# Kernel optimization log

Hardware: AMD Instinct MI355X
Metric: run time of the kernel (lower is better)

The kernel has to match this reference:

```python
import jax, jax.numpy as jnp
import numpy as np

N = 50000      # nodes
E = 800000     # edges (before self-loops)
IN = 256       # input_dim
HID = 72       # hidden_dim
HEADS = 4
NEG_SLOPE = 0.2  # PyG GATConv default leaky-relu slope


def setup_inputs() -> dict:
    key = jax.random.key(0)
    ks = jax.random.split(key, 16)
    rn = lambda k, shape: jax.random.normal(k, shape, jnp.float32) * 0.05
    return {
        "x": jax.random.normal(ks[0], (N, IN), jnp.float32),
        "edge_index": jax.random.randint(ks[1], (2, E), 0, N),
        "W_in": rn(ks[2], (IN, HID)), "b_in": jnp.zeros((HID,), jnp.float32),
        "W1": rn(ks[3], (HID, HEADS * HID)),
        "a_src1": rn(ks[4], (HEADS, HID)), "a_dst1": rn(ks[5], (HEADS, HID)),
        "b1": jnp.zeros((HEADS * HID,), jnp.float32),
        "W2": rn(ks[6], (HEADS * HID, HID)),
        "a_src2": rn(ks[7], (1, HID)), "a_dst2": rn(ks[8], (1, HID)),
        "b2": jnp.zeros((HID,), jnp.float32),
        "W3": rn(ks[9], (HID, HID)),
        "a_src3": rn(ks[10], (1, HID)), "a_dst3": rn(ks[11], (1, HID)),
        "b3": jnp.zeros((HID,), jnp.float32),
        "Ws1": rn(ks[12], (HID, 32)), "bs1": jnp.zeros((32,), jnp.float32),
        "Ws2": rn(ks[13], (32, 1)), "bs2": jnp.zeros((1,), jnp.float32),
    }


def gat_conv(x, src, dst, W, a_src, a_dst, bias, concat):
    # PyG GATConv (eval mode): per-head linear, leaky-relu attention logits,
    # segment softmax over incoming edges per destination, scatter-aggregate.
    H, C = a_src.shape
    h = (x @ W).reshape(-1, H, C)                      # [N, H, C]
    logit_s = jnp.einsum('nhc,hc->nh', h, a_src)       # [N, H]
    logit_d = jnp.einsum('nhc,hc->nh', h, a_dst)       # [N, H]
    e = jax.nn.leaky_relu(logit_s[src] + logit_d[dst], NEG_SLOPE)   # [Et, H]
    emax = jax.ops.segment_max(e, dst, num_segments=N)
    emax = jnp.where(jnp.isfinite(emax), emax, 0.0)
    p = jnp.exp(e - emax[dst])
    denom = jax.ops.segment_sum(p, dst, num_segments=N)
    alpha = p / jnp.maximum(denom[dst], 1e-16)         # [Et, H]
    out = jax.ops.segment_sum(h[src] * alpha[:, :, None], dst, num_segments=N)
    out = out.reshape(-1, H * C) if concat else out.mean(axis=1)
    return out + bias


def reference(x, edge_index, W_in, b_in,
              W1, a_src1, a_dst1, b1,
              W2, a_src2, a_dst2, b2,
              W3, a_src3, a_dst3, b3,
              Ws1, bs1, Ws2, bs2):
    loops = jnp.arange(N)                              # PyG add_self_loops=True
    src = jnp.concatenate([edge_index[0], loops])
    dst = jnp.concatenate([edge_index[1], loops])
    x0 = x @ W_in + b_in                               # [N, HID]
    h = jax.nn.elu(gat_conv(x0, src, dst, W1, a_src1, a_dst1, b1, True))
    h = jax.nn.elu(gat_conv(h, src, dst, W2, a_src2, a_dst2, b2, False))
    h = jax.nn.elu(gat_conv(h, src, dst, W3, a_src3, a_dst3, b3, False))
    h = h + x0
    score = jax.nn.relu(h @ Ws1 + bs1) @ Ws2 + bs2     # dropout = identity (eval)
    return score.squeeze(-1)                           # [N]
```

## Files before the change

### kernel.cpp

```cpp
#include <hip/hip_runtime.h>
#include <hip/hip_fp16.h>
#include <cmath>

#define NN 50000
#define EE 800000
#define ET (EE + NN)
#define IN_DIM 256
#define HID 72
#define CAP 96
#define NRANGE 8
#define RSPAN (NN / NRANGE)
#define SLICE_E 8192

typedef __attribute__((ext_vector_type(8))) short s8v;
typedef __attribute__((ext_vector_type(4))) short s4v;
typedef __attribute__((ext_vector_type(4))) float f4v;
typedef __attribute__((ext_vector_type(2))) float f2v;

__device__ __forceinline__ ushort f2bf(float x) {
    uint u = __float_as_uint(x);
    return (ushort)((u + 0x7fffu + ((u >> 16) & 1u)) >> 16);
}
__device__ __forceinline__ float bf2f(ushort h) {
    return __uint_as_float(((uint)h) << 16);
}
__device__ __forceinline__ void split4(const float4& v, s4v& h, s4v& l) {
    ushort h0 = f2bf(v.x), h1 = f2bf(v.y), h2 = f2bf(v.z), h3 = f2bf(v.w);
    h = (s4v){(short)h0, (short)h1, (short)h2, (short)h3};
    l = (s4v){(short)f2bf(v.x - bf2f(h0)), (short)f2bf(v.y - bf2f(h1)),
              (short)f2bf(v.z - bf2f(h2)), (short)f2bf(v.w - bf2f(h3))};
}
__device__ __forceinline__ f4v mfma16(s8v a, s8v b, f4v c) {
    return __builtin_amdgcn_mfma_f32_16x16x32_bf16(a, b, c, 0, 0, 0);
}
__device__ __forceinline__ f2v unpack_h2(uint pv) {
    __half2 hv = __builtin_bit_cast(__half2, pv);
    return (f2v){__low2float(hv), __high2float(hv)};
}
__device__ __forceinline__ uint pack_h2(float a, float b) {
    __half2 hp = __floats2half2_rn(a, b);
    return __builtin_bit_cast(uint, hp);
}
__device__ __forceinline__ f2v fma2(float w, f2v c, f2v a) {
    return __builtin_elementwise_fma((f2v){w, w}, c, a);
}

__device__ __forceinline__ void wsplit_one(const float* W, int ldw, int K,
        int idx, short* outH, short* outL) {
    int h = idx / (72 * K);
    int rem = idx - h * 72 * K;
    int n = rem / K, k = rem - n * K;
    float v = W[(size_t)k * ldw + h * 72 + n];
    ushort hi = f2bf(v);
    outH[idx] = (short)hi;
    outL[idx] = (short)f2bf(v - bf2f(hi));
}

#define PR0 18432
#define PR1 (PR0 + 20736)
#define PR2 (PR1 + 20736)
#define PR3 (PR2 + 5184)
#define PR4 (PR3 + 288)
#define PRTOT (PR4 + NN)

__global__ __launch_bounds__(256) void prep_kernel(
        const float* __restrict__ W_in, const float* __restrict__ W1,
        const float* __restrict__ W2, const float* __restrict__ W3,
        const float* __restrict__ a_src, const float* __restrict__ a_dst,
        short* __restrict__ BtInH, short* __restrict__ BtInL,
        short* __restrict__ Bt1H, short* __restrict__ Bt1L,
        short* __restrict__ Bt2H, short* __restrict__ Bt2L,
        short* __restrict__ Bt3H, short* __restrict__ Bt3L,
        float* __restrict__ wsrc, float* __restrict__ wdst,
        int* __restrict__ deg, ushort* __restrict__ ell) {
    int gid = blockIdx.x * 256 + threadIdx.x;
    if (gid < PR0) {
        wsplit_one(W_in, 72, 256, gid, BtInH, BtInL);
    } else if (gid < PR1) {
        wsplit_one(W1, 288, 72, gid - PR0, Bt1H, Bt1L);
    } else if (gid < PR2) {
        wsplit_one(W2, 72, 288, gid - PR1, Bt2H, Bt2L);
    } else if (gid < PR3) {
        wsplit_one(W3, 72, 72, gid - PR2, Bt3H, Bt3L);
    } else if (gid < PR4) {
        int j = gid - PR3;
        int h = j / HID, k = j % HID;
        const float* wrow = W1 + (size_t)k * (4 * HID) + h * HID;
        const float* as = a_src + h * HID;
        const float* ad = a_dst + h * HID;
        float s = 0.f, d = 0.f;
        for (int c = 0; c < HID; ++c) {
            float w = wrow[c];
            s = fmaf(w, as[c], s);
            d = fmaf(w, ad[c], d);
        }
        wsrc[j] = s;
        wdst[j] = d;
    } else if (gid < PRTOT) {
        int i = gid - PR4;
        deg[i] = 1;
        ell[(size_t)i * CAP] = (ushort)i;
    }
}

template <int NLOGIT, bool ELU_EPI, bool BATCHED, bool PACKOUT, bool APACK, bool ADJ>
__global__ __launch_bounds__(256) void gemm_mfma(
        const void* __restrict__ Ain, const short* __restrict__ BtH,
        const short* __restrict__ BtL, const float* __restrict__ bias,
        float* __restrict__ C, uint* __restrict__ Cp, int ldp,
        const float* __restrict__ lvs, const float* __restrict__ lvd,
        float* __restrict__ ls, float* __restrict__ ld,
        int M, int K, int lda, int Nfull,
        const int* __restrict__ eiw, int* __restrict__ degw,
        ushort* __restrict__ ellw, int gemmBlocks) {
    __shared__ __align__(16) short AhS[64 * 40], AlS[64 * 40];
    __shared__ __align__(16) short BhS[80 * 40], BlS[80 * 40];

    int tid = threadIdx.x;

    if (ADJ && (int)blockIdx.x >= gemmBlocks) {
        int ab = blockIdx.x - gemmBlocks;
        int slice = ab >> 3;
        int range = blockIdx.x & 7;
        int lo = range * RSPAN;
        int hi = lo + RSPAN;
        #pragma unroll 2
        for (int j = 0; j < 8; ++j) {
            int i0 = slice * SLICE_E + j * 1024 + tid * 4;
            if (i0 >= EE) break;
            int4 d4 = *(const int4*)(eiw + EE + i0);
            int4 s4 = *(const int4*)(eiw + i0);
            int dd[4] = {d4.x, d4.y, d4.z, d4.w};
            int ss[4] = {s4.x, s4.y, s4.z, s4.w};
            #pragma unroll
            for (int u = 0; u < 4; ++u) {
                if (dd[u] >= lo && dd[u] < hi) {
                    int pos = atomicAdd(&degw[dd[u]], 1);
                    if (pos < CAP) ellw[(size_t)dd[u] * CAP + pos] = (ushort)ss[u];
                }
            }
        }
        return;
    }

    int row0 = blockIdx.x * 64;
    int hh = BATCHED ? blockIdx.y : 0;
    int aoff = BATCHED ? hh * (APACK ? 36 : 72) : 0;
    int coff = BATCHED ? hh * 72 : 0;
    const short* bhg = BtH + (size_t)hh * 72 * K;
    const short* blg = BtL + (size_t)hh * 72 * K;

    for (int i = tid; i < 8 * 40; i += 256) {
        BhS[72 * 40 + i] = 0;
        BlS[72 * 40 + i] = 0;
    }

    int w = tid >> 6;
    int lane = tid & 63;
    int q = lane >> 4, l16 = lane & 15;

    f4v acc[5];
    #pragma unroll
    for (int f = 0; f < 5; ++f) acc[f] = (f4v)0.f;

    int ar = tid >> 2;
    int aseg = tid & 3;
    bool arok = (row0 + ar) < M;
    const float* aptrf = nullptr;
    const uint*  aptru = nullptr;
    if constexpr (APACK) {
        aptru = (const uint*)Ain + (size_t)(row0 + ar) * lda + aoff;
    } else {
        aptrf = (const float*)Ain + (size_t)(row0 + ar) * lda + aoff;
    }
    int bn0 = tid >> 2, bq0 = tid & 3;
    int bn1 = (tid + 256) >> 2;

    float4 va, vb;
    s8v bh0, bl0, bh1, bl1;
    auto gload = [&](int k0) {
        va = (float4){0, 0, 0, 0};
        vb = (float4){0, 0, 0, 0};
        int ka = k0 + aseg * 8;
        if constexpr (APACK) {
            if (arok && ka < K) {
                uint4 u = *(const uint4*)(aptru + (ka >> 1));
                f2v p0 = unpack_h2(u.x), p1 = unpack_h2(u.y);
                f2v p2 = unpack_h2(u.z), p3 = unpack_h2(u.w);
                va = (float4){p0.x, p0.y, p1.x, p1.y};
                vb = (float4){p2.x, p2.y, p3.x, p3.y};
            }
        } else {
            if (arok && ka < K)     va = *(const float4*)(aptrf + ka);
            if (arok && ka + 4 < K) vb = *(const float4*)(aptrf + ka + 4);
        }
        bh0 = (s8v)0; bl0 = (s8v)0;
        int kb = k0 + bq0 * 8;
        if (kb < K) {
            bh0 = *(const s8v*)(bhg + (size_t)bn0 * K + kb);
            bl0 = *(const s8v*)(blg + (size_t)bn0 * K + kb);
        }
        bh1 = (s8v)0; bl1 = (s8v)0;
        if (tid < 32 && kb < K) {
            bh1 = *(const s8v*)(bhg + (size_t)bn1 * K + kb);
            bl1 = *(const s8v*)(blg + (size_t)bn1 * K + kb);
        }
    };
    auto commit = [&]() {
        s4v h0, l0, h1, l1;
        split4(va, h0, l0);
        split4(vb, h1, l1);
        *(s4v*)&AhS[ar * 40 + aseg * 8]     = h0;
        *(s4v*)&AhS[ar * 40 + aseg * 8 + 4] = h1;
        *(s4v*)&AlS[ar * 40 + aseg * 8]     = l0;
        *(s4v*)&AlS[ar * 40 + aseg * 8 + 4] = l1;
        *(s8v*)&BhS[bn0 * 40 + bq0 * 8] = bh0;
        *(s8v*)&BlS[bn0 * 40 + bq0 * 8] = bl0;
        if (tid < 32) {
            *(s8v*)&BhS[bn1 * 40 + bq0 * 8] = bh1;
            *(s8v*)&BlS[bn1 * 40 + bq0 * 8] = bl1;
        }
    };

    int ntiles = (K + 31) / 32;
    gload(0);
    for (int t = 0; t < ntiles; ++t) {
        commit();
        __syncthreads();
        if (t + 1 < ntiles) gload((t + 1) * 32);
        s8v ah = *(const s8v*)&AhS[(w * 16 + l16) * 40 + q * 8];
        s8v al = *(const s8v*)&AlS[(w * 16 + l16) * 40 + q * 8];
        #pragma unroll
        for (int f = 0; f < 5; ++f) {
            s8v bh = *(const s8v*)&BhS[(f * 16 + l16) * 40 + q * 8];
            s8v bl = *(const s8v*)&BlS[(f * 16 + l16) * 40 + q * 8];
            acc[f] = mfma16(ah, bh, acc[f]);
            acc[f] = mfma16(ah, bl, acc[f]);
            acc[f] = mfma16(al, bh, acc[f]);
        }
        __syncthreads();
    }

    float v[5][4];
    #pragma unroll
    for (int f = 0; f < 5; ++f) {
        int col = f * 16 + l16;
        bool cv = col < 72;
        #pragma unroll
        for (int r = 0; r < 4; ++r) {
            float t = acc[f][r];
            if (cv && bias) t += bias[coff + col];
            if (ELU_EPI) t = (t > 0.f) ? t : expm1f(t);
            v[f][r] = cv ? t : 0.f;
        }
    }
    if (NLOGIT > 0) {
        #pragma unroll
        for (int h2 = 0; h2 < NLOGIT; ++h2) {
            #pragma unroll
            for (int r = 0; r < 4; ++r) {
                float s = 0.f, d = 0.f;
                #pragma unroll
                for (int f = 0; f < 5; ++f) {
                    int col = f * 16 + l16;
                    float lw = (col < 72) ? lvs[h2 * 72 + col] : 0.f;
                    float dw = (col < 72) ? lvd[h2 * 72 + col] : 0.f;
                    s = fmaf(v[f][r], lw, s);
                    d = fmaf(v[f][r], dw, d);
                }
                s += __shfl_xor(s, 1); s += __shfl_xor(s, 2);
                s += __shfl_xor(s, 4); s += __shfl_xor(s, 8);
                d += __shfl_xor(d, 1); d += __shfl_xor(d, 2);
                d += __shfl_xor(d, 4); d += __shfl_xor(d, 8);
                int gr = row0 + w * 16 + q * 4 + r;
                if (l16 == 0 && gr < M) {
                    ls[gr * NLOGIT + h2] = s;
                    ld[gr * NLOGIT + h2] = d;
                }
            }
        }
    }
    if (PACKOUT) {
        #pragma unroll
        for (int f = 0; f < 5; ++f) {
            int col = f * 16 + l16;
            #pragma unroll
            for (int r = 0; r < 4; ++r) {
                float vo = __shfl_xor(v[f][r], 1);
                if ((l16 & 1) == 0 && col < 72) {
                    int gr = row0 + w * 16 + q * 4 + r;
                    if (gr < M) {
                        Cp[(size_t)gr * ldp + ((coff + col) >> 1)] =
                            pack_h2(v[f][r], vo);
                    }
                }
            }
        }
    }
    if (C != nullptr) {
        #pragma unroll
        for (int f = 0; f < 5; ++f) {
            int col = f * 16 + l16;
            if (col >= 72) continue;
            #pragma unroll
            for (int r = 0; r < 4; ++r) {
                int gr = row0 + w * 16 + q * 4 + r;
                if (gr < M) C[(size_t)gr * Nfull + coff + col] = v[f][r];
            }
        }
    }
}

template <int H, bool EPI, bool ADD_RES, bool POUT>
__global__ __launch_bounds__(64) void agg_gather(
        const uint* __restrict__ featp,
        const float* __restrict__ ls, const float* __restrict__ ld,
        const int* __restrict__ degv, const ushort* __restrict__ ell,
        const float* __restrict__ bias, const float* __restrict__ res,
        float* __restrict__ out, uint* __restrict__ outp, int n) {
    __shared__ float wsh[64 * H];
    __shared__ int ssh[64];
    int wid = blockIdx.x;
    int lane = threadIdx.x;
    int deg = min(degv[wid], CAP);
    const ushort* row = ell + (size_t)wid * CAP;

    float ldh[H];
    if (H == 4) {
        float4 t = ((const float4*)ld)[wid];
        ldh[0] = t.x; ldh[1] = t.y; ldh[2] = t.z; ldh[3] = t.w;
    } else {
        ldh[0] = ld[wid];
    }

    f2v acc2[H];
    #pragma unroll
    for (int h = 0; h < H; ++h) acc2[h] = (f2v)0.f;

    if (deg <= 64) {
        bool act = lane < deg;
        int s = row[act ? lane : 0];
        ssh[lane] = s;
        float e[H];
        float ev[H];
        if (H == 4) {
            float4 lv = ((const float4*)ls)[s];
            ev[0] = lv.x; ev[1] = lv.y; ev[2] = lv.z; ev[3] = lv.w;
        } else {
            ev[0] = ls[s];
        }
        #pragma unroll
        for (int h = 0; h < H; ++h) {
            float vv = ev[h] + ldh[h];
            vv = (vv > 0.f) ? vv : 0.2f * vv;
            e[h] = act ? vv : -__builtin_inff();
        }
        float wv[H];
        #pragma unroll
        for (int h = 0; h < H; ++h) {
            float mh = e[h];
            #pragma unroll
            for (int off = 32; off; off >>= 1) mh = fmaxf(mh, __shfl_xor(mh, off));
            float ph = act ? expf(e[h] - mh) : 0.f;
            float sh = ph;
            #pragma unroll
            for (int off = 32; off; off >>= 1) sh += __shfl_xor(sh, off);
            wv[h] = ph / fmaxf(sh, 1e-16f);
        }
        if (H == 4) {
            ((float4*)wsh)[lane] = (float4){wv[0], wv[1], wv[2], wv[3]};
        } else {
            wsh[lane] = wv[0];
        }
        __syncthreads();

        int nb = (deg + 7) & ~7;
        const uint* rowbase = featp + (lane < 36 ? lane : 0);
        for (int t = 0; t < nb; t += 8) {
            int si[8];
            #pragma unroll
            for (int u = 0; u < 8; ++u) si[u] = ssh[t + u];
            uint pv[8];
            #pragma unroll
            for (int u = 0; u < 8; ++u) pv[u] = rowbase[(size_t)si[u] * 36];
            #pragma unroll
            for (int u = 0; u < 8; ++u) {
                f2v c2 = unpack_h2(pv[u]);
                if constexpr (H == 4) {
                    float4 we = ((const float4*)wsh)[t + u];
                    acc2[0] = fma2(we.x, c2, acc2[0]);
                    acc2[1] = fma2(we.y, c2, acc2[1]);
                    acc2[2] = fma2(we.z, c2, acc2[2]);
                    acc2[3] = fma2(we.w, c2, acc2[3]);
                } else {
                    acc2[0] = fma2(wsh[t + u], c2, acc2[0]);
                }
            }
        }
    } else {
        float m[H];
        #pragma unroll
        for (int h = 0; h < H; ++h) m[h] = -__builtin_inff();
        for (int i = lane; i < deg; i += 64) {
            int s = row[i];
            float e[H];
            if (H == 4) {
                float4 lv = ((const float4*)ls)[s];
                e[0] = lv.x; e[1] = lv.y; e[2] = lv.z; e[3] = lv.w;
            } else {
                e[0] = ls[s];
            }
            #pragma unroll
            for (int h = 0; h < H; ++h) {
                float vv = e[h] + ldh[h];
                vv = (vv > 0.f) ? vv : 0.2f * vv;
                m[h] = fmaxf(m[h], vv);
            }
        }
        #pragma unroll
        for (int h = 0; h < H; ++h)
            #pragma unroll
            for (int off = 32; off; off >>= 1) m[h] = fmaxf(m[h], __shfl_xor(m[h], off));

        float ssum[H];
        #pragma unroll
        for (int h = 0; h < H; ++h) ssum[h] = 0.f;
        for (int i = lane; i < deg; i += 64) {
            int s = row[i];
            float e[H];
            if (H == 4) {
                float4 lv = ((const float4*)ls)[s];
                e[0] = lv.x; e[1] = lv.y; e[2] = lv.z; e[3] = lv.w;
            } else {
                e[0] = ls[s];
            }
            #pragma unroll
            for (int h = 0; h < H; ++h) {
                float vv = e[h] + ldh[h];
                vv = (vv > 0.f) ? vv : 0.2f * vv;
                ssum[h] += expf(vv - m[h]);
            }
        }
        #pragma unroll
        for (int h = 0; h < H; ++h)
            #pragma unroll
            for (int off = 32; off; off >>= 1) ssum[h] += __shfl_xor(ssum[h], off);
        float inv[H];
        #pragma unroll
        for (int h = 0; h < H; ++h) inv[h] = 1.f / fmaxf(ssum[h], 1e-16f);

        for (int base = 0; base < deg; base += 64) {
            int i = base + lane;
            int lim = min(64, deg - base);
            if (i < deg) {
                int s = row[i];
                ssh[lane] = s;
                float e[H];
                if (H == 4) {
                    float4 lv = ((const float4*)ls)[s];
                    e[0] = lv.x; e[1] = lv.y; e[2] = lv.z; e[3] = lv.w;
                } else {
                    e[0] = ls[s];
                }
                if (H == 4) {
                    float p0 = expf(((e[0] + ldh[0] > 0.f) ? e[0] + ldh[0] : 0.2f * (e[0] + ldh[0])) - m[0]) * inv[0];
                    float p1 = expf(((e[1] + ldh[1] > 0.f) ? e[1] + ldh[1] : 0.2f * (e[1] + ldh[1])) - m[1]) * inv[1];
                    float p2 = expf(((e[2] + ldh[2] > 0.f) ? e[2] + ldh[2] : 0.2f * (e[2] + ldh[2])) - m[2]) * inv[2];
                    float p3 = expf(((e[3] + ldh[3] > 0.f) ? e[3] + ldh[3] : 0.2f * (e[3] + ldh[3])) - m[3]) * inv[3];
                    ((float4*)wsh)[lane] = (float4){p0, p1, p2, p3};
                } else {
                    float vv = e[0] + ldh[0];
                    vv = (vv > 0.f) ? vv : 0.2f * vv;
                    wsh[lane] = expf(vv - m[0]) * inv[0];
                }
            }
            __syncthreads();
            for (int t = 0; t < lim; ++t) {
                uint pv = featp[(size_t)ssh[t] * 36 + (lane < 36 ? lane : 0)];
                f2v c2 = unpack_h2(pv);
                if constexpr (H == 4) {
                    float4 we = ((const float4*)wsh)[t];
                    acc2[0] = fma2(we.x, c2, acc2[0]);
                    acc2[1] = fma2(we.y, c2, acc2[1]);
                    acc2[2] = fma2(we.z, c2, acc2[2]);
                    acc2[3] = fma2(we.w, c2, acc2[3]);
                } else {
                    acc2[0] = fma2(wsh[t], c2, acc2[0]);
                }
            }
            __syncthreads();
        }
    }

    if (lane < 36) {
        #pragma unroll
        for (int h = 0; h < H; ++h) {
            float v0 = acc2[h].x, v1 = acc2[h].y;
            if (EPI) {
                v0 += bias[2 * lane];
                v1 += bias[2 * lane + 1];
                v0 = (v0 > 0.f) ? v0 : expm1f(v0);
                v1 = (v1 > 0.f) ? v1 : expm1f(v1);
                if (ADD_RES) {
                    float2 rr = *(const float2*)&res[(size_t)wid * HID + 2 * lane];
                    v0 += rr.x; v1 += rr.y;
                }
            }
            if (POUT) {
                outp[(size_t)wid * (H * 36) + h * 36 + lane] = pack_h2(v0, v1);
            } else {
                *(float2*)&out[(size_t)wid * (H * HID) + h * HID + 2 * lane] =
                    (float2){v0, v1};
            }
        }
    }
}

__global__ __launch_bounds__(256) void score_kernel(
        const float* __restrict__ h, const float* __restrict__ Ws1, const float* __restrict__ bs1,
        const float* __restrict__ Ws2, const float* __restrict__ bs2,
        float* __restrict__ out, int n) {
    int sub = threadIdx.x >> 5;
    int j = threadIdx.x & 31;
    int node = blockIdx.x * 8 + sub;
    if (node >= n) return;
    const float* row = h + (size_t)node * HID;
    float acc = bs1[j];
    #pragma unroll 8
    for (int c = 0; c < HID; ++c) acc = fmaf(row[c], Ws1[c * 32 + j], acc);
    float v = fmaxf(acc, 0.f) * Ws2[j];
    #pragma unroll
    for (int off = 16; off; off >>= 1) v += __shfl_down(v, off, 32);
    if (j == 0) out[node] = v + bs2[0];
}

extern "C" void kernel_launch(void* const* d_in, const int* in_sizes, int n_in,
                              void* d_out, int out_size, void* d_ws, size_t ws_size,
                              hipStream_t stream) {
    const float* x      = (const float*)d_in[0];
    const int*   ei     = (const int*)  d_in[1];
    const float* W_in   = (const float*)d_in[2];
    const float* b_in   = (const float*)d_in[3];
    const float* W1     = (const float*)d_in[4];
    const float* a_src1 = (const float*)d_in[5];
    const float* a_dst1 = (const float*)d_in[6];
    const float* b1     = (const float*)d_in[7];
    const float* W2     = (const float*)d_in[8];
    const float* a_src2 = (const float*)d_in[9];
    const float* a_dst2 = (const float*)d_in[10];
    const float* b2     = (const float*)d_in[11];
    const float* W3     = (const float*)d_in[12];
    const float* a_src3 = (const float*)d_in[13];
    const float* a_dst3 = (const float*)d_in[14];
    const float* b3     = (const float*)d_in[15];
    const float* Ws1    = (const float*)d_in[16];
    const float* bs1    = (const float*)d_in[17];
    const float* Ws2    = (const float*)d_in[18];
    const float* bs2    = (const float*)d_in[19];
    float* out = (float*)d_out;

    float* ws    = (float*)d_ws;
    float* x0    = ws;
    float* h3    = x0 + (size_t)NN * HID;
    float* ls    = h3 + (size_t)NN * HID;
    float* ld    = ls + (size_t)NN * 4;
    float* wsrc1 = ld + (size_t)NN * 4;
    float* wdst1 = wsrc1 + 288;
    int* deg     = (int*)(wdst1 + 288);
    ushort* ell  = (ushort*)(deg + NN);
    uintptr_t bp = ((uintptr_t)(ell + (size_t)NN * CAP) + 15) & ~(uintptr_t)15;
    short* BtInH = (short*)bp;
    short* BtInL = BtInH + 18432;
    short* Bt1H  = BtInL + 18432;
    short* Bt1L  = Bt1H + 20736;
    short* Bt2H  = Bt1L + 20736;
    short* Bt2L  = Bt2H + 20736;
    short* Bt3H  = Bt2L + 20736;
    short* Bt3L  = Bt3H + 5184;
    uint*  x0p   = (uint*)(Bt3L + 5184);
    uint*  a1p   = x0p + (size_t)NN * 36;
    uint*  h1p   = a1p + (size_t)NN * 144;
    uint*  hp2p  = h1p + (size_t)NN * 144;
    uint*  h2p   = hp2p + (size_t)NN * 36;
    uint*  hp3p  = h2p + (size_t)NN * 36;

    prep_kernel<<<(PRTOT + 255) / 256, 256, 0, stream>>>(
        W_in, W1, W2, W3, a_src1, a_dst1,
        BtInH, BtInL, Bt1H, Bt1L, Bt2H, Bt2L, Bt3H, Bt3L, wsrc1, wdst1,
        deg, ell);

    const int mblocks = (NN + 63) / 64;
    const int nslice = (EE + SLICE_E - 1) / SLICE_E;
    const int adjBlocks = nslice * NRANGE;
    gemm_mfma<4, false, false, true, false, true>
        <<<dim3(mblocks + adjBlocks, 1), 256, 0, stream>>>(
        x, BtInH, BtInL, b_in, x0, x0p, 36, wsrc1, wdst1, ls, ld,
        NN, IN_DIM, IN_DIM, HID, ei, deg, ell, mblocks);
    agg_gather<4, false, false, true><<<NN, 64, 0, stream>>>(
        x0p, ls, ld, deg, ell, nullptr, nullptr, nullptr, a1p, NN);
    gemm_mfma<0, true, true, true, true, false><<<dim3(mblocks, 4), 256, 0, stream>>>(
        a1p, Bt1H, Bt1L, b1, nullptr, h1p, 144, nullptr, nullptr, nullptr, nullptr,
        NN, HID, 144, 0, nullptr, nullptr, nullptr, 0);
    gemm_mfma<1, false, false, true, true, false><<<dim3(mblocks, 1), 256, 0, stream>>>(
        h1p, Bt2H, Bt2L, nullptr, nullptr, hp2p, 36, a_src2, a_dst2, ls, ld,
        NN, 288, 144, 0, nullptr, nullptr, nullptr, 0);
    agg_gather<1, true, false, true><<<NN, 64, 0, stream>>>(
        hp2p, ls, ld, deg, ell, b2, nullptr, nullptr, h2p, NN);
    gemm_mfma<1, false, false, true, true, false><<<dim3(mblocks, 1), 256, 0, stream>>>(
        h2p, Bt3H, Bt3L, nullptr, nullptr, hp3p, 36, a_src3, a_dst3, ls, ld,
        NN, HID, 36, 0, nullptr, nullptr, nullptr, 0);
    agg_gather<1, true, true, false><<<NN, 64, 0, stream>>>(
        hp3p, ls, ld, deg, ell, b3, x0, h3, nullptr, NN);
    score_kernel<<<(NN + 7) / 8, 256, 0, stream>>>(h3, Ws1, bs1, Ws2, bs2, out, NN);
}
```

Measured before the change: 372.9 us.

## Fuse score MLP into final aggregation and simplify adjacency build

The final-layer gather kernel now keeps each node's 72-wide output row in shared memory and computes the two-layer score MLP in place. This removes the separate score kernel and the write and read-back of the h3 buffer. The adjacency build inside the first GEMM launch also changes: each thread now handles four edges with direct atomics, replacing the scheme where eight range-partitioned blocks each rescanned every edge slice. That cuts redundant edge-index reads but drops the destination locality grouping of the atomics, and the order of neighbours in the ELL rows will differ between runs.

Result: no change. 366.2 us (-1.8%).

```diff
diff --git a/kernel.cpp b/kernel.cpp
--- a/kernel.cpp
+++ b/kernel.cpp
@@ -8,9 +8,6 @@
 #define IN_DIM 256
 #define HID 72
 #define CAP 96
-#define NRANGE 8
-#define RSPAN (NN / NRANGE)
-#define SLICE_E 8192
 
 typedef __attribute__((ext_vector_type(8))) short s8v;
 typedef __attribute__((ext_vector_type(4))) short s4v;
@@ -119,25 +116,17 @@
     int tid = threadIdx.x;
 
     if (ADJ && (int)blockIdx.x >= gemmBlocks) {
-        int ab = blockIdx.x - gemmBlocks;
-        int slice = ab >> 3;
-        int range = blockIdx.x & 7;
-        int lo = range * RSPAN;
-        int hi = lo + RSPAN;
-        #pragma unroll 2
-        for (int j = 0; j < 8; ++j) {
-            int i0 = slice * SLICE_E + j * 1024 + tid * 4;
-            if (i0 >= EE) break;
+        int t = (blockIdx.x - gemmBlocks) * 256 + tid;
+        int i0 = t * 4;
+        if (i0 < EE) {
+            int4 s4 = *(const int4*)(eiw + i0);
             int4 d4 = *(const int4*)(eiw + EE + i0);
-            int4 s4 = *(const int4*)(eiw + i0);
+            int ss[4] = {s4.x, s4.y, s4.z, s4.w};
             int dd[4] = {d4.x, d4.y, d4.z, d4.w};
-            int ss[4] = {s4.x, s4.y, s4.z, s4.w};
             #pragma unroll
             for (int u = 0; u < 4; ++u) {
-                if (dd[u] >= lo && dd[u] < hi) {
-                    int pos = atomicAdd(&degw[dd[u]], 1);
-                    if (pos < CAP) ellw[(size_t)dd[u] * CAP + pos] = (ushort)ss[u];
-                }
+                int pos = atomicAdd(&degw[dd[u]], 1);
+                if (pos < CAP) ellw[(size_t)dd[u] * CAP + pos] = (ushort)ss[u];
             }
         }
         return;
@@ -311,15 +300,19 @@
     }
 }
 
-template <int H, bool EPI, bool ADD_RES, bool POUT>
+template <int H, bool EPI, bool ADD_RES, bool POUT, bool SCORE>
 __global__ __launch_bounds__(64) void agg_gather(
         const uint* __restrict__ featp,
         const float* __restrict__ ls, const float* __restrict__ ld,
         const int* __restrict__ degv, const ushort* __restrict__ ell,
         const float* __restrict__ bias, const float* __restrict__ res,
-        float* __restrict__ out, uint* __restrict__ outp, int n) {
+        float* __restrict__ out, uint* __restrict__ outp,
+        const float* __restrict__ Ws1, const float* __restrict__ bs1,
+        const float* __restrict__ Ws2, const float* __restrict__ bs2,
+        int n) {
     __shared__ float wsh[64 * H];
     __shared__ int ssh[64];
+    __shared__ float srow[HID];
     int wid = blockIdx.x;
     int lane = threadIdx.x;
     int deg = min(degv[wid], CAP);
@@ -508,30 +501,28 @@
             }
             if (POUT) {
                 outp[(size_t)wid * (H * 36) + h * 36 + lane] = pack_h2(v0, v1);
+            } else if (SCORE) {
+                srow[2 * lane] = v0;
+                srow[2 * lane + 1] = v1;
             } else {
                 *(float2*)&out[(size_t)wid * (H * HID) + h * HID + 2 * lane] =
                     (float2){v0, v1};
             }
         }
     }
-}
-
-__global__ __launch_bounds__(256) void score_kernel(
-        const float* __restrict__ h, const float* __restrict__ Ws1, const float* __restrict__ bs1,
-        const float* __restrict__ Ws2, const float* __restrict__ bs2,
-        float* __restrict__ out, int n) {
-    int sub = threadIdx.x >> 5;
-    int j = threadIdx.x & 31;
-    int node = blockIdx.x * 8 + sub;
-    if (node >= n) return;
-    const float* row = h + (size_t)node * HID;
-    float acc = bs1[j];
-    #pragma unroll 8
-    for (int c = 0; c < HID; ++c) acc = fmaf(row[c], Ws1[c * 32 + j], acc);
-    float v = fmaxf(acc, 0.f) * Ws2[j];
-    #pragma unroll
-    for (int off = 16; off; off >>= 1) v += __shfl_down(v, off, 32);
-    if (j == 0) out[node] = v + bs2[0];
+    if (SCORE) {
+        __syncthreads();
+        if (lane < 32) {
+            float acc = bs1[lane];
+            #pragma unroll 8
+            for (int c = 0; c < HID; ++c)
+                acc = fmaf(srow[c], Ws1[c * 32 + lane], acc);
+            float v = fmaxf(acc, 0.f) * Ws2[lane];
+            #pragma unroll
+            for (int off = 16; off; off >>= 1) v += __shfl_down(v, off, 32);
+            if (lane == 0) out[wid] = v + bs2[0];
+        }
+    }
 }
 
 extern "C" void kernel_launch(void* const* d_in, const int* in_sizes, int n_in,
@@ -561,8 +552,7 @@
 
     float* ws    = (float*)d_ws;
     float* x0    = ws;
-    float* h3    = x0 + (size_t)NN * HID;
-    float* ls    = h3 + (size_t)NN * HID;
+    float* ls    = x0 + (size_t)NN * HID;
     float* ld    = ls + (size_t)NN * 4;
     float* wsrc1 = ld + (size_t)NN * 4;
     float* wdst1 = wsrc1 + 288;
@@ -590,26 +580,27 @@
         deg, ell);
 
     const int mblocks = (NN + 63) / 64;
-    const int nslice = (EE + SLICE_E - 1) / SLICE_E;
-    const int adjBlocks = nslice * NRANGE;
+    const int adjBlocks = (EE / 4 + 255) / 256;
     gemm_mfma<4, false, false, true, false, true>
         <<<dim3(mblocks + adjBlocks, 1), 256, 0, stream>>>(
         x, BtInH, BtInL, b_in, x0, x0p, 36, wsrc1, wdst1, ls, ld,
         NN, IN_DIM, IN_DIM, HID, ei, deg, ell, mblocks);
-    agg_gather<4, false, false, true><<<NN, 64, 0, stream>>>(
-        x0p, ls, ld, deg, ell, nullptr, nullptr, nullptr, a1p, NN);
+    agg_gather<4, false, false, true, false><<<NN, 64, 0, stream>>>(
+        x0p, ls, ld, deg, ell, nullptr, nullptr, nullptr, a1p,
+        nullptr, nullptr, nullptr, nullptr, NN);
     gemm_mfma<0, true, true, true, true, false><<<dim3(mblocks, 4), 256, 0, stream>>>(
         a1p, Bt1H, Bt1L, b1, nullptr, h1p, 144, nullptr, nullptr, nullptr, nullptr,
         NN, HID, 144, 0, nullptr, nullptr, nullptr, 0);
     gemm_mfma<1, false, false, true, true, false><<<dim3(mblocks, 1), 256, 0, stream>>>(
         h1p, Bt2H, Bt2L, nullptr, nullptr, hp2p, 36, a_src2, a_dst2, ls, ld,
         NN, 288, 144, 0, nullptr, nullptr, nullptr, 0);
-    agg_gather<1, true, false, true><<<NN, 64, 0, stream>>>(
-        hp2p, ls, ld, deg, ell, b2, nullptr, nullptr, h2p, NN);
+    agg_gather<1, true, false, true, false><<<NN, 64, 0, stream>>>(
+        hp2p, ls, ld, deg, ell, b2, nullptr, nullptr, h2p,
+        nullptr, nullptr, nullptr, nullptr, NN);
     gemm_mfma<1, false, false, true, true, false><<<dim3(mblocks, 1), 256, 0, stream>>>(
         h2p, Bt3H, Bt3L, nullptr, nullptr, hp3p, 36, a_src3, a_dst3, ls, ld,
         NN, HID, 36, 0, nullptr, nullptr, nullptr, 0);
-    agg_gather<1, true, true, false><<<NN, 64, 0, stream>>>(
-        hp3p, ls, ld, deg, ell, b3, x0, h3, nullptr, NN);
-    score_kernel<<<(NN + 7) / 8, 256, 0, stream>>>(h3, Ws1, bs1, Ws2, bs2, out, NN);
-}
+    agg_gather<1, true, true, false, true><<<NN, 64, 0, stream>>>(
+        hp3p, ls, ld, deg, ell, b3, x0, out, nullptr,
+        Ws1, bs1, Ws2, bs2, NN);
+}
```
